# Optimization experiments

Measured on AMD Instinct MI355X. Metric: run time of the kernel, lower is better.

## Reference

```python
import jax, jax.numpy as jnp
import numpy as np

N_NODES = 2000
LN_EPS = 1e-5
NEG_SLOPE = 0.2  # PyG GATConv default


def _gat(xg, W, b, a_src, a_dst, src, dst):
    # xg: [G, N, Fin]; single-head GATConv, add_self_loops=False
    h = xg @ W                      # [G, N, H]
    es = h @ a_src                  # [G, N]
    ed = h @ a_dst                  # [G, N]
    e = jax.nn.leaky_relu(es[:, src] + ed[:, dst], NEG_SLOPE)  # [G, E]

    def seg_softmax(e_g):
        m = jax.ops.segment_max(e_g, dst, num_segments=N_NODES)
        ex = jnp.exp(e_g - m[dst])
        s = jax.ops.segment_sum(ex, dst, num_segments=N_NODES)
        return ex / (s[dst] + 1e-16)

    alpha = jax.vmap(seg_softmax)(e)            # [G, E]
    msg = alpha[..., None] * h[:, src]          # [G, E, H]
    agg = jax.vmap(lambda m_: jax.ops.segment_sum(m_, dst, num_segments=N_NODES))(msg)
    return agg + b                              # [G, N, H]


def _gcn_layer(x, W, b, a_src, a_dst, src, dst):
    # x: [B, N, T, F] -- faithfully replicate original permute + raw reshape
    B, N, T, F = x.shape
    x_in = jnp.transpose(x, (0, 2, 1, 3)).reshape(B * T, N, F)
    out = _gat(x_in, W, b, a_src, a_dst, src, dst)          # [B*T, N, H]
    out = jax.nn.gelu(out.reshape(B, T, N, -1), approximate=False)
    # original does .reshape(B, N, T, -1) on a [B,T,N,H]-contiguous tensor
    return out.reshape(B, N, T, -1)


def _lstm(x, Wih, Whh, bih, bhh):
    # x: [BN, T, Fin]; torch LSTM gate order i,f,g,o
    BN, T, _ = x.shape
    H = Whh.shape[1]
    xz = x @ Wih.T + (bih + bhh)                # [BN, T, 4H]

    def step(carry, z_t):
        h, c = carry
        z = z_t + h @ Whh.T
        i, f, g, o = jnp.split(z, 4, axis=-1)
        c = jax.nn.sigmoid(f) * c + jax.nn.sigmoid(i) * jnp.tanh(g)
        h = jax.nn.sigmoid(o) * jnp.tanh(c)
        return (h, c), h

    init = (jnp.zeros((BN, H), x.dtype), jnp.zeros((BN, H), x.dtype))
    _, hs = jax.lax.scan(step, init, jnp.swapaxes(xz, 0, 1))
    return jnp.swapaxes(hs, 0, 1)               # [BN, T, H]


def setup_inputs() -> dict:
    key = jax.random.key(0)
    ks = jax.random.split(key, 20)
    B, N, T, NX, H, PL, NY, E = 2, N_NODES, 24, 8, 64, 12, 1, 32000
    p = {}
    p["x"] = jax.random.normal(ks[0], (B, N, T, NX), jnp.float32)
    p["edge_src"] = jax.random.randint(ks[1], (E,), 0, N, jnp.int32)
    p["edge_dst"] = jax.random.randint(ks[2], (E,), 0, N, jnp.int32)
    p["fc_W"] = jax.random.normal(ks[3], (NX, H), jnp.float32) / np.sqrt(NX)
    p["fc_b"] = jnp.zeros((H,), jnp.float32)
    for i, tag in enumerate(["g1", "g2"]):
        p[f"{tag}_W"] = jax.random.normal(ks[4 + 4 * i], (H, H), jnp.float32) / np.sqrt(H)
        p[f"{tag}_b"] = jnp.zeros((H,), jnp.float32)
        p[f"{tag}_asrc"] = jax.random.normal(ks[5 + 4 * i], (H,), jnp.float32) / np.sqrt(H)
        p[f"{tag}_adst"] = jax.random.normal(ks[6 + 4 * i], (H,), jnp.float32) / np.sqrt(H)
    p["lstm_Wih"] = jax.random.normal(ks[12], (4 * H, H), jnp.float32) / np.sqrt(H)
    p["lstm_Whh"] = jax.random.normal(ks[13], (4 * H, H), jnp.float32) / np.sqrt(H)
    p["lstm_bih"] = jnp.zeros((4 * H,), jnp.float32)
    p["lstm_bhh"] = jnp.zeros((4 * H,), jnp.float32)
    p["ln_g"] = jnp.ones((H,), jnp.float32)
    p["ln_b"] = jnp.zeros((H,), jnp.float32)
    p["dense_W"] = jax.random.normal(ks[14], (H, PL * NY), jnp.float32) / np.sqrt(H)
    p["dense_b"] = jnp.zeros((PL * NY,), jnp.float32)
    return p


def reference(x, edge_src, edge_dst, fc_W, fc_b,
              g1_W, g1_b, g1_asrc, g1_adst,
              g2_W, g2_b, g2_asrc, g2_adst,
              lstm_Wih, lstm_Whh, lstm_bih, lstm_bhh,
              ln_g, ln_b, dense_W, dense_b):
    B, N, T, _ = x.shape
    PRED_LEN, NY = 12, 1
    x_h = x @ fc_W + fc_b                                        # [B,N,T,H]
    g1 = _gcn_layer(x_h, g1_W, g1_b, g1_asrc, g1_adst, edge_src, edge_dst)
    g2 = _gcn_layer(g1, g2_W, g2_b, g2_asrc, g2_adst, edge_src, edge_dst)
    H = g2.shape[-1]
    lout = _lstm(g2.reshape(B * N, T, -1), lstm_Wih, lstm_Whh, lstm_bih, lstm_bhh)
    lout = lout.reshape(B, N, T, H)
    mu = jnp.mean(lout, axis=-1, keepdims=True)
    var = jnp.mean(jnp.square(lout - mu), axis=-1, keepdims=True)
    h = (lout - mu) / jnp.sqrt(var + LN_EPS) * ln_g + ln_b
    out = h[:, :, -1:, :] @ dense_W + dense_b                    # [B,N,1,PL*NY]
    return out.reshape(B, N, PRED_LEN, NY)
```

## Files before the change

### kernel.cpp

```cpp
#include <hip/hip_runtime.h>
#include <hip/hip_bf16.h>
#include <math.h>

#define B_   2
#define N_   2000
#define T_   24
#define NX_  8
#define H_   64
#define G_   (B_*T_)
#define E_   32000
#define BN_  (B_*N_)
#define TH_  (T_*H_)
#define NTH_ (N_*T_*H_)
#define GNH_ (G_*N_*H_)
#define NPARAM_ 43340
#define NPARAM_PAD_ 43392
#define LSTM_PAD 72
#define DEGCAP 64

using bf16 = __hip_bfloat16;
typedef short bf16x8 __attribute__((ext_vector_type(8)));
typedef float f32x4  __attribute__((ext_vector_type(4)));

__device__ __forceinline__ float uasf(unsigned u){ return __uint_as_float(u); }
__device__ __forceinline__ float wave_sum(float v){
  #pragma unroll
  for (int o = 32; o > 0; o >>= 1) v += __shfl_xor(v, o, 64);
  return v;
}
__device__ __forceinline__ float fastrcp(float x){ return __builtin_amdgcn_rcpf(x); }
__device__ __forceinline__ float sigf(float x){ return fastrcp(1.f + __expf(-x)); }
__device__ __forceinline__ float tanhfast(float x){ return 1.f - 2.f*fastrcp(1.f + __expf(2.f*x)); }
__device__ __forceinline__ float gelu_exact(float x){ return 0.5f*x*(1.f + erff(x*0.70710678118654752f)); }
__device__ __forceinline__ unsigned f2bf_rtn(float f){
  unsigned u = __float_as_uint(f);
  u += 0x7fffu + ((u >> 16) & 1u);
  return u >> 16;
}
__device__ __forceinline__ bf16x8 pack8(float4 a, float4 b){
  bf16x8 v;
  v[0]=(short)f2bf_rtn(a.x); v[1]=(short)f2bf_rtn(a.y);
  v[2]=(short)f2bf_rtn(a.z); v[3]=(short)f2bf_rtn(a.w);
  v[4]=(short)f2bf_rtn(b.x); v[5]=(short)f2bf_rtn(b.y);
  v[6]=(short)f2bf_rtn(b.z); v[7]=(short)f2bf_rtn(b.w);
  return v;
}

struct ConvArgs {
  const void* src[18];
  int off[19];
};
__global__ __launch_bounds__(256) void prep_kernel(
    ConvArgs a, const unsigned* __restrict__ xw,
    float* __restrict__ dst, int* __restrict__ flag,
    int* __restrict__ cnt_g,
    float* __restrict__ wc, float* __restrict__ bc){
  __shared__ int scnt;
  int tid = threadIdx.x;
  if (tid == 0) scnt = 0;
  __syncthreads();
  int c = 0;
  for (int i = tid; i < 4096; i += 256){
    unsigned e = (xw[i] >> 7) & 0xffu;
    if (e >= 100u && e <= 140u) c++;
  }
  atomicAdd(&scnt, c);
  __syncthreads();
  int isbf = (scnt > 3276) ? 1 : 0;
  int bid = blockIdx.x;

  if (bid < 170){
    if (bid == 0 && tid == 0) *flag = isbf;
    int i = bid*256 + tid;
    if (i < NPARAM_){
      int seg = 0;
      while (i >= a.off[seg+1]) seg++;
      int j = i - a.off[seg];
      float v;
      if (isbf) v = uasf(((unsigned)((const unsigned short*)a.src[seg])[j]) << 16);
      else      v = ((const float*)a.src[seg])[j];
      dst[i] = v;
    }
  } else if (bid == 170){
    for (int i = tid; i < N_; i += 256) cnt_g[i] = 0;
  } else {
    int lane = tid & 63, wave = tid >> 6;
    int b = bid - 171;
    const unsigned short* fcWu = (const unsigned short*)a.src[0];
    const unsigned short* fcbu = (const unsigned short*)a.src[1];
    const unsigned short* g1Wu = (const unsigned short*)a.src[2];
    const float* fcWf = (const float*)a.src[0];
    const float* fcbf = (const float*)a.src[1];
    const float* g1Wf = (const float*)a.src[2];
    #pragma unroll
    for (int s = 0; s < 16; ++s){
      int o = b*64 + wave*16 + s;
      int r = o >> 6;
      int n = o & 63;
      float fa, fb;
      if (isbf){
        fa = (r < 8) ? uasf(((unsigned)fcWu[r*64 + lane]) << 16)
                     : uasf(((unsigned)fcbu[lane]) << 16);
        fb = uasf(((unsigned)g1Wu[lane*64 + n]) << 16);
      } else {
        fa = (r < 8) ? fcWf[r*64 + lane] : fcbf[lane];
        fb = g1Wf[lane*64 + n];
      }
      float sv = wave_sum(fa * fb);
      if (lane == 0){
        if (r < 8) wc[r*64 + n] = sv;
        else       bc[n] = sv;
      }
    }
  }
}

__global__ __launch_bounds__(256) void gat_h1_fused_kernel(
    const void* __restrict__ xraw, const int* __restrict__ flag,
    const int* __restrict__ esrc, const int* __restrict__ edst,
    int* __restrict__ cnt_g, int* __restrict__ slot,
    const float* __restrict__ wc, const float* __restrict__ bc,
    const float* __restrict__ asrc, const float* __restrict__ adst,
    unsigned short* __restrict__ hbuf, float* __restrict__ es, float* __restrict__ ed){
  if (blockIdx.x < 125){
    int e = blockIdx.x*256 + threadIdx.x;
    int d = edst[e];
    int pos = atomicAdd(&cnt_g[d], 1);
    if (pos < DEGCAP) slot[(d << 6) + pos] = esrc[e];
  }
  int lane = threadIdx.x & 63, wave = threadIdx.x >> 6;
  int q = lane >> 4, c = lane & 15;
  int isbf = *flag;
  bf16x8 Bf[4];
  #pragma unroll
  for (int nt = 0; nt < 4; ++nt){
    bf16x8 v;
    #pragma unroll
    for (int j = 0; j < 8; ++j)
      v[j] = (q == 0) ? (short)f2bf_rtn(wc[j*64 + nt*16 + c]) : (short)0;
    Bf[nt] = v;
  }
  float bcv[4];
  #pragma unroll
  for (int nt = 0; nt < 4; ++nt) bcv[nt] = bc[nt*16 + c];
  float aS[4], aD[4];
  #pragma unroll
  for (int nt = 0; nt < 4; ++nt){ aS[nt] = asrc[nt*16+c]; aD[nt] = adst[nt*16+c]; }

  int w = blockIdx.x*4 + wave;
  #pragma unroll
  for (int it = 0; it < 2; ++it){
    int tile = w*2 + it;
    int p0 = tile*16;
    int g  = p0 / N_, n0 = p0 - g*N_;
    int bb = g / T_,  tt = g - bb*T_;
    bf16x8 A0;
    #pragma unroll
    for (int j = 0; j < 8; ++j) A0[j] = 0;
    if (q == 0){
      size_t rowelt = ((size_t)(bb*N_ + n0 + c)*T_ + tt)*NX_;
      if (isbf){
        A0 = *(const bf16x8*)((const unsigned short*)xraw + rowelt);
      } else {
        const float4* xr4 = (const float4*)((const float*)xraw + rowelt);
        A0 = pack8(xr4[0], xr4[1]);
      }
    }
    f32x4 acc[4];
    #pragma unroll
    for (int nt = 0; nt < 4; ++nt){ acc[nt][0]=bcv[nt]; acc[nt][1]=bcv[nt]; acc[nt][2]=bcv[nt]; acc[nt][3]=bcv[nt]; }
    #pragma unroll
    for (int nt = 0; nt < 4; ++nt) acc[nt] = __builtin_amdgcn_mfma_f32_16x16x32_bf16(A0, Bf[nt], acc[nt], 0, 0, 0);

    #pragma unroll
    for (int nt = 0; nt < 4; ++nt){
      #pragma unroll
      for (int r = 0; r < 4; ++r)
        hbuf[(size_t)(p0 + q*4 + r)*H_ + nt*16 + c] = (unsigned short)f2bf_rtn(acc[nt][r]);
    }
    #pragma unroll
    for (int r = 0; r < 4; ++r){
      float e1 = acc[0][r]*aS[0] + acc[1][r]*aS[1] + acc[2][r]*aS[2] + acc[3][r]*aS[3];
      float e2 = acc[0][r]*aD[0] + acc[1][r]*aD[1] + acc[2][r]*aD[2] + acc[3][r]*aD[3];
      #pragma unroll
      for (int o = 8; o > 0; o >>= 1){
        e1 += __shfl_xor(e1, o, 64);
        e2 += __shfl_xor(e2, o, 64);
      }
      if (c == 0){
        es[p0 + q*4 + r] = e1;
        ed[p0 + q*4 + r] = e2;
      }
    }
  }
}

__global__ __launch_bounds__(256) void gat_h2_mfma_kernel(
    const unsigned short* __restrict__ xinb, const float* __restrict__ W,
    const float* __restrict__ asrc, const float* __restrict__ adst,
    unsigned short* __restrict__ hbuf, float* __restrict__ es, float* __restrict__ ed){
  int lane = threadIdx.x & 63, wave = threadIdx.x >> 6;
  int q = lane >> 4, c = lane & 15;
  bf16x8 Bf[4][2];
  #pragma unroll
  for (int nt = 0; nt < 4; ++nt){
    #pragma unroll
    for (int ks = 0; ks < 2; ++ks){
      bf16x8 v;
      #pragma unroll
      for (int j = 0; j < 8; ++j)
        v[j] = (short)f2bf_rtn(W[(ks*32 + q*8 + j)*H_ + nt*16 + c]);
      Bf[nt][ks] = v;
    }
  }
  float aS[4], aD[4];
  #pragma unroll
  for (int nt = 0; nt < 4; ++nt){ aS[nt] = asrc[nt*16+c]; aD[nt] = adst[nt*16+c]; }

  int w = blockIdx.x*4 + wave;
  #pragma unroll
  for (int it = 0; it < 2; ++it){
    int tile = w*2 + it;
    int p0 = tile*16;
    int p  = p0 + c;
    int g = p / N_, n = p - g*N_;
    int bb = g / T_, t = g - bb*T_;
    const unsigned short* xr = xinb + (size_t)bb*NTH_ + (size_t)n*TH_ + (size_t)t*H_;
    bf16x8 A0 = *(const bf16x8*)(xr + q*8);
    bf16x8 A1 = *(const bf16x8*)(xr + 32 + q*8);

    f32x4 acc[4];
    #pragma unroll
    for (int nt = 0; nt < 4; ++nt){ acc[nt][0]=0.f; acc[nt][1]=0.f; acc[nt][2]=0.f; acc[nt][3]=0.f; }
    #pragma unroll
    for (int nt = 0; nt < 4; ++nt) acc[nt] = __builtin_amdgcn_mfma_f32_16x16x32_bf16(A0, Bf[nt][0], acc[nt], 0, 0, 0);
    #pragma unroll
    for (int nt = 0; nt < 4; ++nt) acc[nt] = __builtin_amdgcn_mfma_f32_16x16x32_bf16(A1, Bf[nt][1], acc[nt], 0, 0, 0);

    #pragma unroll
    for (int nt = 0; nt < 4; ++nt){
      #pragma unroll
      for (int r = 0; r < 4; ++r)
        hbuf[(size_t)(p0 + q*4 + r)*H_ + nt*16 + c] = (unsigned short)f2bf_rtn(acc[nt][r]);
    }
    #pragma unroll
    for (int r = 0; r < 4; ++r){
      float e1 = acc[0][r]*aS[0] + acc[1][r]*aS[1] + acc[2][r]*aS[2] + acc[3][r]*aS[3];
      float e2 = acc[0][r]*aD[0] + acc[1][r]*aD[1] + acc[2][r]*aD[2] + acc[3][r]*aD[3];
      #pragma unroll
      for (int o = 8; o > 0; o >>= 1){
        e1 += __shfl_xor(e1, o, 64);
        e2 += __shfl_xor(e2, o, 64);
      }
      if (c == 0){
        es[p0 + q*4 + r] = e1;
        ed[p0 + q*4 + r] = e2;
      }
    }
  }
}

__global__ __launch_bounds__(256) void gat_agg_kernel(
    const unsigned short* __restrict__ hbuf, const float* __restrict__ es, const float* __restrict__ ed,
    const int* __restrict__ cnt_g, const int* __restrict__ slot,
    const float* __restrict__ bias, unsigned short* __restrict__ goutb){
  int lane = threadIdx.x & 63, wave = threadIdx.x >> 6;
  int qd = lane >> 4, ln = lane & 15;
  int gd = (blockIdx.x*4 + wave)*4 + qd;
  int g = gd / N_, d = gd - g*N_;
  int start = d << 6;
  int deg = min(cnt_g[d], DEGCAP);
  const float* esg = es + (size_t)g*N_;
  float edv = ed[(size_t)g*N_ + d];
  const char* hg = (const char*)(hbuf + (size_t)g*N_*H_);
  unsigned lanoff = ((unsigned)ln) << 3;
  int hbase = qd << 4;
  int dm = deg;
  dm = max(dm, __shfl_xor(dm, 16, 64));
  dm = max(dm, __shfl_xor(dm, 32, 64));
  int NC = (dm + 15) >> 4;

  int svk[4]; float sck[4];
  #pragma unroll
  for (int k = 0; k < 4; ++k){ svk[k] = 0; sck[k] = -1e30f; }
  #pragma unroll
  for (int k = 0; k < 4; ++k){
    int i = k*16 + ln;
    if (k < NC && i < deg) svk[k] = slot[start + i];
  }
  #pragma unroll
  for (int k = 0; k < 4; ++k){
    int i = k*16 + ln;
    if (k < NC && i < deg){
      float e = esg[svk[k]] + edv;
      sck[k] = e > 0.f ? e : 0.2f*e;
    }
  }
  float m = fmaxf(fmaxf(sck[0], sck[1]), fmaxf(sck[2], sck[3]));
  #pragma unroll
  for (int o = 8; o > 0; o >>= 1) m = fmaxf(m, __shfl_xor(m, o, 64));
  float exk[4]; float ssum = 0.f;
  #pragma unroll
  for (int k = 0; k < 4; ++k){
    int i = k*16 + ln;
    float e = (k < NC && i < deg) ? __expf(sck[k] - m) : 0.f;
    exk[k] = e; ssum += e;
  }
  #pragma unroll
  for (int o = 8; o > 0; o >>= 1) ssum += __shfl_xor(ssum, o, 64);
  float inv = fastrcp(ssum + 1e-16f);
  unsigned pwk[4];
  #pragma unroll
  for (int k = 0; k < 4; ++k)
    pwk[k] = (f2bf_rtn(exk[k]*inv) << 16) | (unsigned)svk[k];

  float a0 = 0.f, a1 = 0.f, a2 = 0.f, a3 = 0.f;
  for (int k = 0; k < NC; ++k){
    unsigned pw = pwk[k];
    int myrem = deg - k*16;
    int remw = dm - k*16; if (remw > 16) remw = 16;
    for (int j0 = 0; j0 < remw; j0 += 8){
      unsigned wv[8]; float aa[8]; unsigned off[8];
      #pragma unroll
      for (int u = 0; u < 8; ++u){
        int j = j0 + u;
        wv[u] = (unsigned)__shfl((int)pw, hbase + j, 64);
        aa[u] = (j < myrem) ? uasf(wv[u] & 0xffff0000u) : 0.f;
        off[u] = ((wv[u] & 0xffffu) << 7) + lanoff;
      }
      uint2 hv[8];
      #pragma unroll
      for (int u = 0; u < 8; ++u)
        hv[u] = *(const uint2*)(hg + off[u]);
      #pragma unroll
      for (int u = 0; u < 8; ++u){
        a0 = fmaf(aa[u], uasf(hv[u].x << 16), a0);
        a1 = fmaf(aa[u], uasf(hv[u].x & 0xffff0000u), a1);
        a2 = fmaf(aa[u], uasf(hv[u].y << 16), a2);
        a3 = fmaf(aa[u], uasf(hv[u].y & 0xffff0000u), a3);
      }
    }
  }
  float4 bv = ((const float4*)bias)[ln];
  uint2 ov;
  ov.x = f2bf_rtn(gelu_exact(a0 + bv.x)) | (f2bf_rtn(gelu_exact(a1 + bv.y)) << 16);
  ov.y = f2bf_rtn(gelu_exact(a2 + bv.z)) | (f2bf_rtn(gelu_exact(a3 + bv.w)) << 16);
  ((uint2*)(goutb + (size_t)gd*H_))[ln] = ov;
}

__global__ __launch_bounds__(256) void lstm_final_kernel(
    const unsigned short* __restrict__ xinb,
    const float* __restrict__ Wih,
    const float* __restrict__ Whh,
    const float* __restrict__ bih, const float* __restrict__ bhh,
    const float* __restrict__ lng, const float* __restrict__ lnb,
    const float* __restrict__ dW, const float* __restrict__ db,
    const int* __restrict__ flag, void* __restrict__ outv){
  __shared__ __align__(16) unsigned short Hlds[2][16*LSTM_PAD];
  __shared__ float smH[16][68];
  int tid = threadIdx.x;
  int lane = tid & 63, wave = tid >> 6;
  int q = lane >> 4, c = lane & 15;
  int s0 = blockIdx.x * 16;

  bf16x8 Bf[4][4];
  #pragma unroll
  for (int g = 0; g < 4; ++g){
    int n = g*64 + wave*16 + c;
    #pragma unroll
    for (int ks = 0; ks < 4; ++ks){
      const float* srcp = (ks < 2) ? (Whh + (size_t)n*64 + ks*32 + q*8)
                                   : (Wih + (size_t)n*64 + (ks-2)*32 + q*8);
      float4 a = ((const float4*)srcp)[0];
      float4 b = ((const float4*)srcp)[1];
      Bf[g][ks] = pack8(a, b);
    }
  }
  float bsum[4];
  #pragma unroll
  for (int g = 0; g < 4; ++g){
    int n = g*64 + wave*16 + c;
    bsum[g] = bih[n] + bhh[n];
  }
  for (int i = tid; i < 16*LSTM_PAD; i += 256) Hlds[0][i] = 0;
  float cst[4] = {0.f, 0.f, 0.f, 0.f};
  __syncthreads();

  int buf = 0;
  for (int t = 0; t < T_; ++t){
    const unsigned short* xr = xinb + ((size_t)(s0 + c)*T_ + t)*64;
    bf16x8 Ax0 = *(const bf16x8*)(xr + q*8);
    bf16x8 Ax1 = *(const bf16x8*)(xr + 32 + q*8);
    const bf16x8* hrow = (const bf16x8*)(Hlds[buf] + c*LSTM_PAD);
    bf16x8 Ah0 = hrow[q];
    bf16x8 Ah1 = hrow[4 + q];

    f32x4 acc[4];
    #pragma unroll
    for (int g = 0; g < 4; ++g){ acc[g][0]=bsum[g]; acc[g][1]=bsum[g]; acc[g][2]=bsum[g]; acc[g][3]=bsum[g]; }
    #pragma unroll
    for (int g = 0; g < 4; ++g) acc[g] = __builtin_amdgcn_mfma_f32_16x16x32_bf16(Ah0, Bf[g][0], acc[g], 0, 0, 0);
    #pragma unroll
    for (int g = 0; g < 4; ++g) acc[g] = __builtin_amdgcn_mfma_f32_16x16x32_bf16(Ah1, Bf[g][1], acc[g], 0, 0, 0);
    #pragma unroll
    for (int g = 0; g < 4; ++g) acc[g] = __builtin_amdgcn_mfma_f32_16x16x32_bf16(Ax0, Bf[g][2], acc[g], 0, 0, 0);
    #pragma unroll
    for (int g = 0; g < 4; ++g) acc[g] = __builtin_amdgcn_mfma_f32_16x16x32_bf16(Ax1, Bf[g][3], acc[g], 0, 0, 0);

    float hv[4];
    #pragma unroll
    for (int r = 0; r < 4; ++r){
      float zi = acc[0][r], zf = acc[1][r], zg = acc[2][r], zo = acc[3][r];
      cst[r] = sigf(zf)*cst[r] + sigf(zi)*tanhfast(zg);
      hv[r] = sigf(zo)*tanhfast(cst[r]);
    }
    if (t == T_-1){
      #pragma unroll
      for (int r = 0; r < 4; ++r)
        smH[q*4 + r][wave*16 + c] = hv[r];
    } else {
      #pragma unroll
      for (int r = 0; r < 4; ++r)
        Hlds[buf^1][(q*4 + r)*LSTM_PAD + wave*16 + c] = (unsigned short)f2bf_rtn(hv[r]);
      __syncthreads();
      buf ^= 1;
    }
  }
  __syncthreads();

  int isbf = *flag;
  #pragma unroll
  for (int si = 0; si < 4; ++si){
    int s = wave*4 + si;
    float h = smH[s][lane];
    float mu = wave_sum(h) * (1.f/64.f);
    float dev = h - mu;
    float var = wave_sum(dev*dev) * (1.f/64.f);
    float hn = dev * rsqrtf(var + 1e-5f) * lng[lane] + lnb[lane];
    smH[s][lane] = hn;
    if (lane < 12){
      float o = db[lane];
      #pragma unroll
      for (int k = 0; k < 64; ++k) o = fmaf(smH[s][k], dW[k*12 + lane], o);
      size_t oi = (size_t)(s0 + s)*12 + lane;
      if (isbf) ((unsigned short*)outv)[oi] = (unsigned short)f2bf_rtn(o);
      else      ((float*)outv)[oi] = o;
    }
  }
}

extern "C" void kernel_launch(void* const* d_in, const int* in_sizes, int n_in,
                              void* d_out, int out_size, void* d_ws, size_t ws_size,
                              hipStream_t stream) {
  const int* esrc = (const int*)d_in[1];
  const int* edst = (const int*)d_in[2];

  static const int sizes[18] = {512, 64, 4096, 64, 64, 64, 4096, 64, 64, 64,
                                16384, 16384, 256, 256, 64, 64, 768, 12};
  static const int srcidx[18] = {3, 4, 5, 6, 7, 8, 9, 10, 11, 12,
                                 13, 14, 15, 16, 17, 18, 19, 20};
  ConvArgs ca;
  {
    int acc = 0;
    for (int i = 0; i < 18; ++i){ ca.src[i] = d_in[srcidx[i]]; ca.off[i] = acc; acc += sizes[i]; }
    ca.off[18] = acc;
  }

  float* P     = (float*)d_ws;
  float* bufA  = P + NPARAM_PAD_;
  float* bufB  = bufA + (size_t)GNH_/2 + 64;
  float* esb   = bufB + (size_t)GNH_/2 + 64;
  float* edb   = esb  + (size_t)G_*N_;
  int*   cnt_g = (int*)(edb + (size_t)G_*N_);
  int*   slot  = cnt_g + N_;
  int*   flag  = slot + N_*DEGCAP;
  float* wcb   = (float*)(flag + 1);
  unsigned short* goutb = (unsigned short*)bufA;
  unsigned short* hbuf  = (unsigned short*)bufB;

  const float* pg1b = P + 4672;
  const float* pg1as= P + 4736;
  const float* pg1ad= P + 4800;
  const float* pg2W = P + 4864;
  const float* pg2b = P + 8960;
  const float* pg2as= P + 9024;
  const float* pg2ad= P + 9088;
  const float* pWih = P + 9152;
  const float* pWhh = P + 25536;
  const float* pbih = P + 41920;
  const float* pbhh = P + 42176;
  const float* plng = P + 42432;
  const float* plnb = P + 42496;
  const float* pdW  = P + 42560;
  const float* pdb  = P + 43328;

  prep_kernel<<<180, 256, 0, stream>>>(ca, (const unsigned*)d_in[0],
                                       P, flag, cnt_g, wcb, wcb + 512);

  gat_h1_fused_kernel<<<750, 256, 0, stream>>>(d_in[0], flag, esrc, edst, cnt_g, slot,
                                               wcb, wcb + 512, pg1as, pg1ad, hbuf, esb, edb);
  gat_agg_kernel<<<6000, 256, 0, stream>>>(hbuf, esb, edb, cnt_g, slot, pg1b, goutb);

  gat_h2_mfma_kernel<<<750, 256, 0, stream>>>(goutb, pg2W, pg2as, pg2ad, hbuf, esb, edb);
  gat_agg_kernel<<<6000, 256, 0, stream>>>(hbuf, esb, edb, cnt_g, slot, pg2b, goutb);

  lstm_final_kernel<<<250, 256, 0, stream>>>(goutb, pWih, pWhh, pbih, pbhh,
                                             plng, plnb, pdW, pdb, flag, d_out);
}
```

Baseline: 218.2 us.

## Remap GAT aggregation to 8 lanes per node with 16-byte gathers

The aggregation kernel now gives each destination node 8 lanes instead of 16, so each wave covers 8 nodes and each lane gathers 16 bytes (8 bf16 features) per neighbour instead of 8 bytes. The grid is halved to match. A fast path keeps softmax weights in registers for degree up to 32. Higher degrees take a three-pass fallback that recomputes the scores on each pass. The aim is fewer, wider memory transactions and less shuffle and reduction overhead per node, at the cost of more registers per lane and less parallelism for high-degree nodes.

Measured after the change: 224.9 us. 3.1% more time.

```diff
diff --git a/kernel.cpp b/kernel.cpp
--- a/kernel.cpp
+++ b/kernel.cpp
@@ -265,87 +265,153 @@
     const int* __restrict__ cnt_g, const int* __restrict__ slot,
     const float* __restrict__ bias, unsigned short* __restrict__ goutb){
   int lane = threadIdx.x & 63, wave = threadIdx.x >> 6;
-  int qd = lane >> 4, ln = lane & 15;
-  int gd = (blockIdx.x*4 + wave)*4 + qd;
+  int g3 = lane >> 3, ln = lane & 7;
+  int gd = (blockIdx.x*4 + wave)*8 + g3;
   int g = gd / N_, d = gd - g*N_;
   int start = d << 6;
   int deg = min(cnt_g[d], DEGCAP);
   const float* esg = es + (size_t)g*N_;
   float edv = ed[(size_t)g*N_ + d];
   const char* hg = (const char*)(hbuf + (size_t)g*N_*H_);
-  unsigned lanoff = ((unsigned)ln) << 3;
-  int hbase = qd << 4;
+  unsigned lanoff = ((unsigned)ln) << 4;
+  int hbase = g3 << 3;
   int dm = deg;
+  dm = max(dm, __shfl_xor(dm, 8, 64));
   dm = max(dm, __shfl_xor(dm, 16, 64));
   dm = max(dm, __shfl_xor(dm, 32, 64));
-  int NC = (dm + 15) >> 4;
-
-  int svk[4]; float sck[4];
-  #pragma unroll
-  for (int k = 0; k < 4; ++k){ svk[k] = 0; sck[k] = -1e30f; }
-  #pragma unroll
-  for (int k = 0; k < 4; ++k){
-    int i = k*16 + ln;
-    if (k < NC && i < deg) svk[k] = slot[start + i];
-  }
-  #pragma unroll
-  for (int k = 0; k < 4; ++k){
-    int i = k*16 + ln;
-    if (k < NC && i < deg){
-      float e = esg[svk[k]] + edv;
-      sck[k] = e > 0.f ? e : 0.2f*e;
-    }
-  }
-  float m = fmaxf(fmaxf(sck[0], sck[1]), fmaxf(sck[2], sck[3]));
-  #pragma unroll
-  for (int o = 8; o > 0; o >>= 1) m = fmaxf(m, __shfl_xor(m, o, 64));
-  float exk[4]; float ssum = 0.f;
-  #pragma unroll
-  for (int k = 0; k < 4; ++k){
-    int i = k*16 + ln;
-    float e = (k < NC && i < deg) ? __expf(sck[k] - m) : 0.f;
-    exk[k] = e; ssum += e;
-  }
-  #pragma unroll
-  for (int o = 8; o > 0; o >>= 1) ssum += __shfl_xor(ssum, o, 64);
-  float inv = fastrcp(ssum + 1e-16f);
-  unsigned pwk[4];
-  #pragma unroll
-  for (int k = 0; k < 4; ++k)
-    pwk[k] = (f2bf_rtn(exk[k]*inv) << 16) | (unsigned)svk[k];
-
-  float a0 = 0.f, a1 = 0.f, a2 = 0.f, a3 = 0.f;
-  for (int k = 0; k < NC; ++k){
-    unsigned pw = pwk[k];
-    int myrem = deg - k*16;
-    int remw = dm - k*16; if (remw > 16) remw = 16;
-    for (int j0 = 0; j0 < remw; j0 += 8){
+
+  float a0=0.f,a1=0.f,a2=0.f,a3=0.f,a4=0.f,a5=0.f,a6=0.f,a7=0.f;
+  if (dm <= 32){
+    int NC = (dm + 7) >> 3;
+    int svk[4]; float sck[4];
+    #pragma unroll
+    for (int k = 0; k < 4; ++k){ svk[k] = 0; sck[k] = -1e30f; }
+    #pragma unroll
+    for (int k = 0; k < 4; ++k){
+      int i = k*8 + ln;
+      if (k < NC && i < deg) svk[k] = slot[start + i];
+    }
+    #pragma unroll
+    for (int k = 0; k < 4; ++k){
+      int i = k*8 + ln;
+      if (k < NC && i < deg){
+        float e = esg[svk[k]] + edv;
+        sck[k] = e > 0.f ? e : 0.2f*e;
+      }
+    }
+    float m = fmaxf(fmaxf(sck[0], sck[1]), fmaxf(sck[2], sck[3]));
+    #pragma unroll
+    for (int o = 4; o > 0; o >>= 1) m = fmaxf(m, __shfl_xor(m, o, 64));
+    float exk[4]; float ssum = 0.f;
+    #pragma unroll
+    for (int k = 0; k < 4; ++k){
+      int i = k*8 + ln;
+      float e = (k < NC && i < deg) ? __expf(sck[k] - m) : 0.f;
+      exk[k] = e; ssum += e;
+    }
+    #pragma unroll
+    for (int o = 4; o > 0; o >>= 1) ssum += __shfl_xor(ssum, o, 64);
+    float inv = fastrcp(ssum + 1e-16f);
+    unsigned pwk[4];
+    #pragma unroll
+    for (int k = 0; k < 4; ++k)
+      pwk[k] = (f2bf_rtn(exk[k]*inv) << 16) | (unsigned)svk[k];
+
+    for (int k = 0; k < NC; ++k){
+      unsigned pw = pwk[k];
+      int myrem = deg - k*8;
       unsigned wv[8]; float aa[8]; unsigned off[8];
       #pragma unroll
       for (int u = 0; u < 8; ++u){
-        int j = j0 + u;
-        wv[u] = (unsigned)__shfl((int)pw, hbase + j, 64);
-        aa[u] = (j < myrem) ? uasf(wv[u] & 0xffff0000u) : 0.f;
+        wv[u] = (unsigned)__shfl((int)pw, hbase + u, 64);
+        aa[u] = (u < myrem) ? uasf(wv[u] & 0xffff0000u) : 0.f;
         off[u] = ((wv[u] & 0xffffu) << 7) + lanoff;
       }
-      uint2 hv[8];
+      uint4 hv[8];
       #pragma unroll
       for (int u = 0; u < 8; ++u)
-        hv[u] = *(const uint2*)(hg + off[u]);
+        hv[u] = *(const uint4*)(hg + off[u]);
       #pragma unroll
       for (int u = 0; u < 8; ++u){
         a0 = fmaf(aa[u], uasf(hv[u].x << 16), a0);
         a1 = fmaf(aa[u], uasf(hv[u].x & 0xffff0000u), a1);
         a2 = fmaf(aa[u], uasf(hv[u].y << 16), a2);
         a3 = fmaf(aa[u], uasf(hv[u].y & 0xffff0000u), a3);
-      }
-    }
-  }
-  float4 bv = ((const float4*)bias)[ln];
-  uint2 ov;
-  ov.x = f2bf_rtn(gelu_exact(a0 + bv.x)) | (f2bf_rtn(gelu_exact(a1 + bv.y)) << 16);
-  ov.y = f2bf_rtn(gelu_exact(a2 + bv.z)) | (f2bf_rtn(gelu_exact(a3 + bv.w)) << 16);
-  ((uint2*)(goutb + (size_t)gd*H_))[ln] = ov;
+        a4 = fmaf(aa[u], uasf(hv[u].z << 16), a4);
+        a5 = fmaf(aa[u], uasf(hv[u].z & 0xffff0000u), a5);
+        a6 = fmaf(aa[u], uasf(hv[u].w << 16), a6);
+        a7 = fmaf(aa[u], uasf(hv[u].w & 0xffff0000u), a7);
+      }
+    }
+  } else {
+    float m = -1e30f;
+    for (int base = 0; base < deg; base += 8){
+      int i = base + ln;
+      if (i < deg){
+        int s = slot[start + i];
+        float e = esg[s] + edv;
+        float t = e > 0.f ? e : 0.2f*e;
+        m = fmaxf(m, t);
+      }
+    }
+    #pragma unroll
+    for (int o = 4; o > 0; o >>= 1) m = fmaxf(m, __shfl_xor(m, o, 64));
+    float ssum = 0.f;
+    for (int base = 0; base < deg; base += 8){
+      int i = base + ln;
+      if (i < deg){
+        int s = slot[start + i];
+        float e = esg[s] + edv;
+        float t = e > 0.f ? e : 0.2f*e;
+        ssum += __expf(t - m);
+      }
+    }
+    #pragma unroll
+    for (int o = 4; o > 0; o >>= 1) ssum += __shfl_xor(ssum, o, 64);
+    float inv = fastrcp(ssum + 1e-16f);
+    for (int base = 0; base < dm; base += 8){
+      int i = base + ln;
+      int sv = 0; float ex = 0.f;
+      if (i < deg){
+        sv = slot[start + i];
+        float e = esg[sv] + edv;
+        float t = e > 0.f ? e : 0.2f*e;
+        ex = __expf(t - m) * inv;
+      }
+      unsigned pw = (f2bf_rtn(ex) << 16) | (unsigned)sv;
+      int myrem = deg - base;
+      unsigned wv[8]; float aa[8]; unsigned off[8];
+      #pragma unroll
+      for (int u = 0; u < 8; ++u){
+        wv[u] = (unsigned)__shfl((int)pw, hbase + u, 64);
+        aa[u] = (u < myrem) ? uasf(wv[u] & 0xffff0000u) : 0.f;
+        off[u] = ((wv[u] & 0xffffu) << 7) + lanoff;
+      }
+      uint4 hv[8];
+      #pragma unroll
+      for (int u = 0; u < 8; ++u)
+        hv[u] = *(const uint4*)(hg + off[u]);
+      #pragma unroll
+      for (int u = 0; u < 8; ++u){
+        a0 = fmaf(aa[u], uasf(hv[u].x << 16), a0);
+        a1 = fmaf(aa[u], uasf(hv[u].x & 0xffff0000u), a1);
+        a2 = fmaf(aa[u], uasf(hv[u].y << 16), a2);
+        a3 = fmaf(aa[u], uasf(hv[u].y & 0xffff0000u), a3);
+        a4 = fmaf(aa[u], uasf(hv[u].z << 16), a4);
+        a5 = fmaf(aa[u], uasf(hv[u].z & 0xffff0000u), a5);
+        a6 = fmaf(aa[u], uasf(hv[u].w << 16), a6);
+        a7 = fmaf(aa[u], uasf(hv[u].w & 0xffff0000u), a7);
+      }
+    }
+  }
+  float4 bv0 = ((const float4*)bias)[ln*2];
+  float4 bv1 = ((const float4*)bias)[ln*2 + 1];
+  uint4 ov;
+  ov.x = f2bf_rtn(gelu_exact(a0 + bv0.x)) | (f2bf_rtn(gelu_exact(a1 + bv0.y)) << 16);
+  ov.y = f2bf_rtn(gelu_exact(a2 + bv0.z)) | (f2bf_rtn(gelu_exact(a3 + bv0.w)) << 16);
+  ov.z = f2bf_rtn(gelu_exact(a4 + bv1.x)) | (f2bf_rtn(gelu_exact(a5 + bv1.y)) << 16);
+  ov.w = f2bf_rtn(gelu_exact(a6 + bv1.z)) | (f2bf_rtn(gelu_exact(a7 + bv1.w)) << 16);
+  ((uint4*)(goutb + (size_t)gd*H_))[ln] = ov;
 }
 
 __global__ __launch_bounds__(256) void lstm_final_kernel(
@@ -499,10 +565,10 @@
 
   gat_h1_fused_kernel<<<750, 256, 0, stream>>>(d_in[0], flag, esrc, edst, cnt_g, slot,
                                                wcb, wcb + 512, pg1as, pg1ad, hbuf, esb, edb);
-  gat_agg_kernel<<<6000, 256, 0, stream>>>(hbuf, esb, edb, cnt_g, slot, pg1b, goutb);
+  gat_agg_kernel<<<3000, 256, 0, stream>>>(hbuf, esb, edb, cnt_g, slot, pg1b, goutb);
 
   gat_h2_mfma_kernel<<<750, 256, 0, stream>>>(goutb, pg2W, pg2as, pg2ad, hbuf, esb, edb);
-  gat_agg_kernel<<<6000, 256, 0, stream>>>(hbuf, esb, edb, cnt_g, slot, pg2b, goutb);
+  gat_agg_kernel<<<3000, 256, 0, stream>>>(hbuf, esb, edb, cnt_g, slot, pg2b, goutb);
 
   lstm_final_kernel<<<250, 256, 0, stream>>>(goutb, pWih, pWhh, pbih, pbhh,
                                              plng, plnb, pdW, pdb, flag, d_out);
```
